# Performance work log

Hardware: AMD Instinct MI355X
Metric: run time of the kernel (lower is better)

## Reference

```python
import jax, jax.numpy as jnp
import numpy as np

B, P, D, N, K = 8, 784, 1536, 20000, 9


def setup_inputs() -> dict:
    key = jax.random.key(0)
    k1, k2 = jax.random.split(key)
    x = jax.random.normal(k1, (B, P, D), dtype=jnp.float32)       # patch embeddings [B, P, D]
    memory = jax.random.normal(k2, (N, D), dtype=jnp.float32)     # FAISS memory bank [N, D]
    return {"x": x, "memory": memory, "k": K}


def reference(x, memory, k):
    # Squared L2 distances (FAISS IndexFlatL2 convention): [B, P, N]
    x2 = jnp.sum(x * x, axis=-1, keepdims=True)                   # [B, P, 1]
    m2 = jnp.sum(memory * memory, axis=-1)                        # [N]
    d = x2 + m2[None, None, :] - 2.0 * jnp.einsum('bpd,nd->bpn', x, memory)
    # k nearest (smallest distances, ascending) -> score_patches [B, P, k]
    neg_topk, _ = jax.lax.top_k(-d, k)
    score_patches = -neg_topk
    closest_dist = score_patches[..., 0]                          # [B, P]
    idxmax = jnp.argmax(closest_dist, axis=1)                     # [B]
    # N_b: the k neighbor distances of the worst (max closest-dist) patch
    N_b = jnp.take_along_axis(score_patches, idxmax[:, None, None], axis=1)[:, 0, :]  # [B, k]
    N_b = N_b - jnp.max(N_b, axis=1, keepdims=True)               # numerical stabilization (as in source)
    N_b_exp = jnp.exp(N_b)
    w = 1.0 - jnp.max(N_b_exp, axis=1) / jnp.sum(N_b_exp, axis=1)  # [B]
    score = w * jnp.max(closest_dist, axis=1)                      # [B]
    return score
```

## Files before the change

### kernel.cpp

```cpp
#include <hip/hip_runtime.h>
#include <hip/hip_fp8.h>
#include <math.h>

#define B_    8
#define P_    784
#define M_    6272
#define D_    1536
#define N_    20000
#define NC_   8

#define MPAD  6400
#define NPAD2 20224
#define MT2   25
#define NT2   79
#define KT2   12

#define NBLK  625

using i32x8  = __attribute__((ext_vector_type(8))) int;
using f32x4v = __attribute__((ext_vector_type(4))) float;

#define GLD_LDS16(src, dst)                                            \
  __builtin_amdgcn_global_load_lds(                                    \
      (__attribute__((address_space(1))) const void*)(src),            \
      (__attribute__((address_space(3))) void*)(dst), 16, 0, 0)

__device__ __forceinline__ unsigned char f2fp8(float v) {
  __hip_fp8_e4m3 q(v);
  return (unsigned char)q.__x;
}

__device__ __forceinline__ unsigned fenc(float f) {
  unsigned u = __float_as_uint(f);
  return (u >> 31) ? ~u : (u | 0x80000000u);
}
__device__ __forceinline__ float fdec(unsigned k) {
  return (k >> 31) ? __uint_as_float(k & 0x7FFFFFFFu) : __uint_as_float(~k);
}

__device__ __forceinline__ void convert_one(const float* __restrict__ src,
                                            unsigned char* __restrict__ dst,
                                            float* __restrict__ sq,
                                            int row, int realrows) {
  const int t = threadIdx.x;
  if (row >= realrows) {
    unsigned* w = (unsigned*)(dst + (size_t)row * D_);
    for (int i = t; i < D_ / 4; i += 256) w[i] = 0u;
    if (t == 0) sq[row] = 1e30f;
    return;
  }
  const float4* r4 = (const float4*)(src + (size_t)row * D_);
  unsigned* w = (unsigned*)(dst + (size_t)row * D_);
  float s = 0.f;
  for (int i = t; i < D_ / 4; i += 256) {
    float4 v = r4[i];
    s += v.x * v.x + v.y * v.y + v.z * v.z + v.w * v.w;
    unsigned pk = (unsigned)f2fp8(v.x) | ((unsigned)f2fp8(v.y) << 8) |
                  ((unsigned)f2fp8(v.z) << 16) | ((unsigned)f2fp8(v.w) << 24);
    w[i] = pk;
  }
#pragma unroll
  for (int m = 32; m >= 1; m >>= 1) s += __shfl_xor(s, m);
  __shared__ float ws4[4];
  if ((t & 63) == 0) ws4[t >> 6] = s;
  __syncthreads();
  if (t == 0) sq[row] = ws4[0] + ws4[1] + ws4[2] + ws4[3];
}

__global__ void convert_all(const float* __restrict__ x, const float* __restrict__ mem,
                            unsigned char* __restrict__ xq, unsigned char* __restrict__ mq,
                            float* __restrict__ x2, float* __restrict__ m2) {
  const int blk = blockIdx.x;
  if (blk < NPAD2) convert_one(mem, mq, m2, blk, N_);
  else convert_one(x, xq, x2, blk - NPAD2, M_);
}

__global__ __launch_bounds__(512, 2) void gemm_min8(
    const unsigned char* __restrict__ xq, const unsigned char* __restrict__ mq,
    const float* __restrict__ m2, unsigned* __restrict__ closest_enc) {
  __shared__ __attribute__((aligned(16))) char ldsFlat[131072];
  __shared__ float ldsMin[4][256];

  const int NWG = MT2 * NT2;
  const int bid = blockIdx.x;
  const int q = NWG >> 3, r = NWG & 7;
  const int xcd = bid & 7, loc = bid >> 3;
  const int wg = (xcd < r ? xcd * (q + 1) : r * (q + 1) + (xcd - r) * q) + loc;
  const int s = wg / (5 * NT2);
  const int r2 = wg - s * (5 * NT2);
  const int mT = s * 5 + (r2 % 5);
  const int nT = r2 / 5;

  const int tid = threadIdx.x;
  const int lane = tid & 63, wid = tid >> 6;
  const int wm = wid >> 2, wn = wid & 3;
  const int g = lane >> 4, r16 = lane & 15;
  const int mBase = mT * 256, nBase = nT * 256;

  const int stRow = wid * 8 + (lane >> 3);
  const int stA = mBase + stRow;
  const int stB = nBase + stRow;
  const int cswz16 = ((lane & 7) ^ ((lane >> 3) & 7)) * 16;

  const int csl = (g * 32) ^ ((r16 & 7) << 4);
  const int csh = csl ^ 16;
  const int rdA = wm * 16384 + r16 * 128;
  const int rdB = wn * 8192 + r16 * 128;

#define STAGE(matsel, srcp, rowb, bufb, h, ktv) do {                        \
    char* dst_ = ldsFlat + (matsel) * 65536 + (bufb) * 32768 +              \
                 (h) * 16384 + wid * 1024;                                  \
    const unsigned char* s_ =                                               \
        (srcp) + (size_t)((rowb) + (h) * 128) * 1536 + (ktv) * 128 + cswz16;\
    GLD_LDS16(s_, dst_);                                                    \
    GLD_LDS16(s_ + 64 * 1536, dst_ + 8192);                                 \
  } while (0)

#define LDFRAG(base, off) ({                                                \
    int4 lo_ = *(const int4*)((base) + (off) + csl);                        \
    int4 hi_ = *(const int4*)((base) + (off) + csh);                        \
    i32x8{lo_.x, lo_.y, lo_.z, lo_.w, hi_.x, hi_.y, hi_.z, hi_.w}; })

#define MFMA8(a, b, c) __builtin_amdgcn_mfma_scale_f32_16x16x128_f8f6f4(    \
    (a), (b), (c), 0, 0, 0, 0x7F7F7F7F, 0, 0x7F7F7F7F)

  f32x4v acc[8][4];
#pragma unroll
  for (int i = 0; i < 8; ++i)
#pragma unroll
    for (int j = 0; j < 4; ++j) acc[i][j] = f32x4v{0.f, 0.f, 0.f, 0.f};

  STAGE(1, mq, stB, 0, 0, 0);
  STAGE(1, mq, stB, 0, 1, 0);
  STAGE(0, xq, stA, 0, 0, 0);
  STAGE(0, xq, stA, 0, 1, 0);
  STAGE(1, mq, stB, 1, 0, 1);
  STAGE(1, mq, stB, 1, 1, 1);
  asm volatile("s_waitcnt vmcnt(4)");
  __builtin_amdgcn_s_barrier();
  __builtin_amdgcn_sched_barrier(0);

#pragma unroll 1
  for (int kt = 0; kt < KT2; ++kt) {
    const int bufc = kt & 1;
    const char* Ab = ldsFlat + bufc * 32768;
    const char* Bb = ldsFlat + 65536 + bufc * 32768;
    const bool stgA = (kt + 1) < KT2;
    const bool stgB = (kt + 2) < KT2;
    i32x8 bf[4], af[4];

#pragma unroll
    for (int nf = 0; nf < 4; ++nf) bf[nf] = LDFRAG(Bb, rdB + nf * 2048);
#pragma unroll
    for (int mf = 0; mf < 4; ++mf) af[mf] = LDFRAG(Ab, rdA + mf * 2048);
    if (stgA) {
      STAGE(0, xq, stA, bufc ^ 1, 0, kt + 1);
      STAGE(0, xq, stA, bufc ^ 1, 1, kt + 1);
    }
    __builtin_amdgcn_s_barrier();
    asm volatile("s_waitcnt lgkmcnt(0)");
    __builtin_amdgcn_s_setprio(1);
#pragma unroll
    for (int mf = 0; mf < 4; ++mf)
#pragma unroll
      for (int nf = 0; nf < 4; ++nf)
        acc[mf][nf] = MFMA8(af[mf], bf[nf], acc[mf][nf]);
    __builtin_amdgcn_s_setprio(0);
    __builtin_amdgcn_s_barrier();

#pragma unroll
    for (int mf = 0; mf < 4; ++mf) af[mf] = LDFRAG(Ab, rdA + (mf + 4) * 2048);
    if (stgB) {
      STAGE(1, mq, stB, bufc, 0, kt + 2);
      STAGE(1, mq, stB, bufc, 1, kt + 2);
    }
    __builtin_amdgcn_s_barrier();
    asm volatile("s_waitcnt lgkmcnt(0)");
    __builtin_amdgcn_s_setprio(1);
#pragma unroll
    for (int mf = 0; mf < 4; ++mf)
#pragma unroll
      for (int nf = 0; nf < 4; ++nf)
        acc[mf + 4][nf] = MFMA8(af[mf], bf[nf], acc[mf + 4][nf]);
    __builtin_amdgcn_s_setprio(0);
    if (kt >= KT2 - 2) {
      asm volatile("s_waitcnt vmcnt(0)");
    } else {
      asm volatile("s_waitcnt vmcnt(4)");
    }
    __builtin_amdgcn_s_barrier();
    __builtin_amdgcn_sched_barrier(0);
  }
#undef STAGE
#undef LDFRAG
#undef MFMA8

  float m2v[4];
#pragma unroll
  for (int nf = 0; nf < 4; ++nf) m2v[nf] = m2[nBase + wn * 64 + nf * 16 + r16];
#pragma unroll
  for (int mf = 0; mf < 8; ++mf) {
    float mn[4];
#pragma unroll
    for (int i = 0; i < 4; ++i) {
      float v = m2v[0] - 2.f * acc[mf][0][i];
      v = fminf(v, m2v[1] - 2.f * acc[mf][1][i]);
      v = fminf(v, m2v[2] - 2.f * acc[mf][2][i]);
      v = fminf(v, m2v[3] - 2.f * acc[mf][3][i]);
      mn[i] = v;
    }
#pragma unroll
    for (int msk = 1; msk < 16; msk <<= 1)
#pragma unroll
      for (int i = 0; i < 4; ++i) mn[i] = fminf(mn[i], __shfl_xor(mn[i], msk));
    if (r16 == 0)
#pragma unroll
      for (int i = 0; i < 4; ++i)
        ldsMin[wn][wm * 128 + mf * 16 + g * 4 + i] = mn[i];
  }
  __syncthreads();
  if (tid < 256) {
    float v = fminf(fminf(ldsMin[0][tid], ldsMin[1][tid]),
                    fminf(ldsMin[2][tid], ldsMin[3][tid]));
    atomicMin(&closest_enc[mBase + tid], fenc(v));
  }
}

__global__ void topcand_kernel(const unsigned* __restrict__ closest_enc,
                               const float* __restrict__ x2,
                               int* __restrict__ cand) {
  const int b = blockIdx.x;
  const int t = threadIdx.x;
  __shared__ float cls[P_];
  for (int p = t; p < P_; p += 256) {
    const int row = b * P_ + p;
    cls[p] = x2[row] + fdec(closest_enc[row]);
  }
  __syncthreads();
  __shared__ float wv[4];
  __shared__ int wi_[4];
  __shared__ int picked[NC_];
  for (int r = 0; r < NC_; ++r) {
    float mv = -3e38f; int mi = 1 << 30;
    for (int p = t; p < P_; p += 256) {
      bool skip = false;
      for (int c = 0; c < r; ++c) skip |= (picked[c] == p);
      float v = cls[p];
      if (!skip && (v > mv || (v == mv && p < mi))) { mv = v; mi = p; }
    }
#pragma unroll
    for (int m = 32; m >= 1; m >>= 1) {
      float ov = __shfl_xor(mv, m); int oi = __shfl_xor(mi, m);
      if (ov > mv || (ov == mv && oi < mi)) { mv = ov; mi = oi; }
    }
    if ((t & 63) == 0) { wv[t >> 6] = mv; wi_[t >> 6] = mi; }
    __syncthreads();
    if (t == 0) {
      float bv = wv[0]; int bi = wi_[0];
      for (int w = 1; w < 4; ++w)
        if (wv[w] > bv || (wv[w] == bv && wi_[w] < bi)) { bv = wv[w]; bi = wi_[w]; }
      picked[r] = bi;
      cand[b * NC_ + r] = bi;
    }
    __syncthreads();
  }
}

__device__ __forceinline__ void ins9(float* t, float v) {
  if (v < t[8]) {
    int p = 8;
    while (p > 0 && t[p - 1] > v) { t[p] = t[p - 1]; --p; }
    t[p] = v;
  }
}

__global__ __launch_bounds__(256) void cand_dist9(
    const float* __restrict__ x, const float* __restrict__ mem,
    const float* __restrict__ x2, const float* __restrict__ m2,
    const int* __restrict__ cand, float* __restrict__ ctop) {
  const int wid = threadIdx.x >> 6, lane = threadIdx.x & 63;
  const int blk = blockIdx.x;
  __shared__ float ldsD[B_ * NC_][36];

  for (int batch = 0; batch < 2; ++batch) {
    const int rbase = blk * 32 + wid * 8 + batch * 4;
    float4 m4[4][6];
    float m2r[4];
#pragma unroll
    for (int k = 0; k < 4; ++k) {
      const float4* mrow = (const float4*)(mem + (size_t)(rbase + k) * D_);
#pragma unroll
      for (int j = 0; j < 6; ++j) m4[k][j] = mrow[j * 64 + lane];
      m2r[k] = m2[rbase + k];
    }
    for (int bc = 0; bc < B_ * NC_; ++bc) {
      const int b = bc / NC_;
      const int p = cand[bc];
      const float4* xp = (const float4*)(x + ((size_t)b * P_ + p) * D_);
      float s0 = 0.f, s1 = 0.f, s2 = 0.f, s3 = 0.f;
#pragma unroll
      for (int j = 0; j < 6; ++j) {
        float4 a = xp[j * 64 + lane];
        s0 += a.x * m4[0][j].x + a.y * m4[0][j].y + a.z * m4[0][j].z + a.w * m4[0][j].w;
        s1 += a.x * m4[1][j].x + a.y * m4[1][j].y + a.z * m4[1][j].z + a.w * m4[1][j].w;
        s2 += a.x * m4[2][j].x + a.y * m4[2][j].y + a.z * m4[2][j].z + a.w * m4[2][j].w;
        s3 += a.x * m4[3][j].x + a.y * m4[3][j].y + a.z * m4[3][j].z + a.w * m4[3][j].w;
      }
#pragma unroll
      for (int msk = 32; msk >= 1; msk >>= 1) {
        s0 += __shfl_xor(s0, msk); s1 += __shfl_xor(s1, msk);
        s2 += __shfl_xor(s2, msk); s3 += __shfl_xor(s3, msk);
      }
      if (lane == 0) {
        const float xx = x2[b * P_ + p];
        const int rloc = wid * 8 + batch * 4;
        ldsD[bc][rloc + 0] = xx + m2r[0] - 2.f * s0;
        ldsD[bc][rloc + 1] = xx + m2r[1] - 2.f * s1;
        ldsD[bc][rloc + 2] = xx + m2r[2] - 2.f * s2;
        ldsD[bc][rloc + 3] = xx + m2r[3] - 2.f * s3;
      }
    }
  }
  __syncthreads();
  if (lane < 16) {
    const int bc = wid * 16 + lane;
    float t[9];
#pragma unroll
    for (int i = 0; i < 9; ++i) t[i] = 3e38f;
    for (int i = 0; i < 32; ++i) ins9(t, ldsD[bc][i]);
    float* o = ctop + ((size_t)bc * NBLK + blk) * 9;
#pragma unroll
    for (int i = 0; i < 9; ++i) o[i] = t[i];
  }
}

__global__ void merge_top9(const float* __restrict__ ctop, float* __restrict__ top9) {
  const int bc = blockIdx.x;
  const float* d = ctop + (size_t)bc * (NBLK * 9);
  float t[9];
#pragma unroll
  for (int i = 0; i < 9; ++i) t[i] = 3e38f;
  for (int n = threadIdx.x; n < NBLK * 9; n += 256) ins9(t, d[n]);
  __shared__ float l9[256 * 9];
  __shared__ float l9b[32 * 9];
  for (int i = 0; i < 9; ++i) l9[threadIdx.x * 9 + i] = t[i];
  __syncthreads();
  if (threadIdx.x < 32) {
    float u[9];
#pragma unroll
    for (int i = 0; i < 9; ++i) u[i] = 3e38f;
    for (int s = 0; s < 8; ++s)
      for (int i = 0; i < 9; ++i) ins9(u, l9[(threadIdx.x * 8 + s) * 9 + i]);
    for (int i = 0; i < 9; ++i) l9b[threadIdx.x * 9 + i] = u[i];
  }
  __syncthreads();
  if (threadIdx.x == 0) {
    float u[9];
#pragma unroll
    for (int i = 0; i < 9; ++i) u[i] = 3e38f;
    for (int s = 0; s < 32; ++s)
      for (int i = 0; i < 9; ++i) ins9(u, l9b[s * 9 + i]);
    for (int i = 0; i < 9; ++i) top9[bc * 9 + i] = u[i];
  }
}

__global__ void score_kernel(const float* __restrict__ top9, const int* __restrict__ cand,
                             float* __restrict__ out) {
  const int b = threadIdx.x;
  if (b >= B_) return;
  float bestv = -3e38f; int bestc = 0, bestp = 1 << 30;
  for (int c = 0; c < NC_; ++c) {
    float v = top9[(b * NC_ + c) * 9 + 0];
    int p = cand[b * NC_ + c];
    if (v > bestv || (v == bestv && p < bestp)) { bestv = v; bestc = c; bestp = p; }
  }
  const float* v9 = &top9[(b * NC_ + bestc) * 9];
  float mx = v9[8];
  float sum = 0.f, mxe = 0.f;
  for (int i = 0; i < 9; ++i) {
    float e = expf(v9[i] - mx);
    sum += e;
    if (e > mxe) mxe = e;
  }
  out[b] = (1.f - mxe / sum) * bestv;
}

extern "C" void kernel_launch(void* const* d_in, const int* in_sizes, int n_in,
                              void* d_out, int out_size, void* d_ws, size_t ws_size,
                              hipStream_t stream) {
  const float* x = (const float*)d_in[0];
  const float* mem = (const float*)d_in[1];
  float* out = (float*)d_out;
  char* ws = (char*)d_ws;

  unsigned char* xq    = (unsigned char*)(ws);
  unsigned char* mq    = (unsigned char*)(ws + 9830400);
  float* x2            = (float*)(ws + 40894464);
  float* m2            = (float*)(ws + 40920064);
  unsigned* closest_enc= (unsigned*)(ws + 41000960);
  int*   cand          = (int*)  (ws + 41026560);
  float* ctop          = (float*)(ws + 41026816);
  float* top9          = (float*)(ws + 42466816);

  hipMemsetAsync(closest_enc, 0xFF, MPAD * 4, stream);
  convert_all<<<NPAD2 + MPAD, 256, 0, stream>>>(x, mem, xq, mq, x2, m2);
  gemm_min8<<<MT2 * NT2, 512, 0, stream>>>(xq, mq, m2, closest_enc);
  topcand_kernel<<<B_, 256, 0, stream>>>(closest_enc, x2, cand);
  cand_dist9<<<NBLK, 256, 0, stream>>>(x, mem, x2, m2, cand, ctop);
  merge_top9<<<B_ * NC_, 256, 0, stream>>>(ctop, top9);
  score_kernel<<<1, 64, 0, stream>>>(top9, cand, out);
}
```

Baseline: 494.5 us.

## Use hardware fp8 pack, fold memset into convert, fuse merge and score

Replaces the per-element fp8 conversion with the packed hardware convert builtin. Folds the closest_enc memset into the convert kernel and merges the top-9 merge and score kernels into one per-batch kernel, removing two launches. Restructures cand_dist9 so each wave holds 8 memory rows in registers at once, so candidate rows are read once instead of twice. In exchange, the fused merge runs only 8 blocks that loop over candidates serially, and cand_dist9 uses more registers.

```diff
diff --git a/kernel.cpp b/kernel.cpp
--- a/kernel.cpp
+++ b/kernel.cpp
@@ -1,5 +1,4 @@
 #include <hip/hip_runtime.h>
-#include <hip/hip_fp8.h>
 #include <math.h>
 
 #define B_    8
@@ -24,11 +23,6 @@
   __builtin_amdgcn_global_load_lds(                                    \
       (__attribute__((address_space(1))) const void*)(src),            \
       (__attribute__((address_space(3))) void*)(dst), 16, 0, 0)
-
-__device__ __forceinline__ unsigned char f2fp8(float v) {
-  __hip_fp8_e4m3 q(v);
-  return (unsigned char)q.__x;
-}
 
 __device__ __forceinline__ unsigned fenc(float f) {
   unsigned u = __float_as_uint(f);
@@ -55,9 +49,9 @@
   for (int i = t; i < D_ / 4; i += 256) {
     float4 v = r4[i];
     s += v.x * v.x + v.y * v.y + v.z * v.z + v.w * v.w;
-    unsigned pk = (unsigned)f2fp8(v.x) | ((unsigned)f2fp8(v.y) << 8) |
-                  ((unsigned)f2fp8(v.z) << 16) | ((unsigned)f2fp8(v.w) << 24);
-    w[i] = pk;
+    int pk = __builtin_amdgcn_cvt_pk_fp8_f32(v.x, v.y, 0, false);
+    pk     = __builtin_amdgcn_cvt_pk_fp8_f32(v.z, v.w, pk, true);
+    w[i] = (unsigned)pk;
   }
 #pragma unroll
   for (int m = 32; m >= 1; m >>= 1) s += __shfl_xor(s, m);
@@ -69,8 +63,11 @@
 
 __global__ void convert_all(const float* __restrict__ x, const float* __restrict__ mem,
                             unsigned char* __restrict__ xq, unsigned char* __restrict__ mq,
-                            float* __restrict__ x2, float* __restrict__ m2) {
+                            float* __restrict__ x2, float* __restrict__ m2,
+                            unsigned* __restrict__ closest_enc) {
   const int blk = blockIdx.x;
+  if (blk < MPAD / 256)
+    closest_enc[blk * 256 + threadIdx.x] = 0xFFFFFFFFu;
   if (blk < NPAD2) convert_one(mem, mq, m2, blk, N_);
   else convert_one(x, xq, x2, blk - NPAD2, M_);
 }
@@ -282,43 +279,40 @@
   const int blk = blockIdx.x;
   __shared__ float ldsD[B_ * NC_][36];
 
-  for (int batch = 0; batch < 2; ++batch) {
-    const int rbase = blk * 32 + wid * 8 + batch * 4;
-    float4 m4[4][6];
-    float m2r[4];
-#pragma unroll
-    for (int k = 0; k < 4; ++k) {
-      const float4* mrow = (const float4*)(mem + (size_t)(rbase + k) * D_);
-#pragma unroll
-      for (int j = 0; j < 6; ++j) m4[k][j] = mrow[j * 64 + lane];
-      m2r[k] = m2[rbase + k];
-    }
-    for (int bc = 0; bc < B_ * NC_; ++bc) {
-      const int b = bc / NC_;
-      const int p = cand[bc];
-      const float4* xp = (const float4*)(x + ((size_t)b * P_ + p) * D_);
-      float s0 = 0.f, s1 = 0.f, s2 = 0.f, s3 = 0.f;
-#pragma unroll
-      for (int j = 0; j < 6; ++j) {
-        float4 a = xp[j * 64 + lane];
-        s0 += a.x * m4[0][j].x + a.y * m4[0][j].y + a.z * m4[0][j].z + a.w * m4[0][j].w;
-        s1 += a.x * m4[1][j].x + a.y * m4[1][j].y + a.z * m4[1][j].z + a.w * m4[1][j].w;
-        s2 += a.x * m4[2][j].x + a.y * m4[2][j].y + a.z * m4[2][j].z + a.w * m4[2][j].w;
-        s3 += a.x * m4[3][j].x + a.y * m4[3][j].y + a.z * m4[3][j].z + a.w * m4[3][j].w;
-      }
-#pragma unroll
-      for (int msk = 32; msk >= 1; msk >>= 1) {
-        s0 += __shfl_xor(s0, msk); s1 += __shfl_xor(s1, msk);
-        s2 += __shfl_xor(s2, msk); s3 += __shfl_xor(s3, msk);
-      }
-      if (lane == 0) {
-        const float xx = x2[b * P_ + p];
-        const int rloc = wid * 8 + batch * 4;
-        ldsD[bc][rloc + 0] = xx + m2r[0] - 2.f * s0;
-        ldsD[bc][rloc + 1] = xx + m2r[1] - 2.f * s1;
-        ldsD[bc][rloc + 2] = xx + m2r[2] - 2.f * s2;
-        ldsD[bc][rloc + 3] = xx + m2r[3] - 2.f * s3;
-      }
+  const int rbase = blk * 32 + wid * 8;
+  float4 m4[8][6];
+  float m2r[8];
+#pragma unroll
+  for (int k = 0; k < 8; ++k) {
+    const float4* mrow = (const float4*)(mem + (size_t)(rbase + k) * D_);
+#pragma unroll
+    for (int j = 0; j < 6; ++j) m4[k][j] = mrow[j * 64 + lane];
+    m2r[k] = m2[rbase + k];
+  }
+#pragma unroll 2
+  for (int bc = 0; bc < B_ * NC_; ++bc) {
+    const int b = bc / NC_;
+    const int p = cand[bc];
+    const float4* xp = (const float4*)(x + ((size_t)b * P_ + p) * D_);
+    float s[8];
+#pragma unroll
+    for (int k = 0; k < 8; ++k) s[k] = 0.f;
+#pragma unroll
+    for (int j = 0; j < 6; ++j) {
+      float4 a = xp[j * 64 + lane];
+#pragma unroll
+      for (int k = 0; k < 8; ++k)
+        s[k] += a.x * m4[k][j].x + a.y * m4[k][j].y + a.z * m4[k][j].z + a.w * m4[k][j].w;
+    }
+#pragma unroll
+    for (int msk = 32; msk >= 1; msk >>= 1)
+#pragma unroll
+      for (int k = 0; k < 8; ++k) s[k] += __shfl_xor(s[k], msk);
+    if (lane == 0) {
+      const float xx = x2[b * P_ + p];
+#pragma unroll
+      for (int k = 0; k < 8; ++k)
+        ldsD[bc][wid * 8 + k] = xx + m2r[k] - 2.f * s[k];
     }
   }
   __syncthreads();
@@ -334,55 +328,57 @@
   }
 }
 
-__global__ void merge_top9(const float* __restrict__ ctop, float* __restrict__ top9) {
-  const int bc = blockIdx.x;
-  const float* d = ctop + (size_t)bc * (NBLK * 9);
-  float t[9];
-#pragma unroll
-  for (int i = 0; i < 9; ++i) t[i] = 3e38f;
-  for (int n = threadIdx.x; n < NBLK * 9; n += 256) ins9(t, d[n]);
+__global__ void merge_score(const float* __restrict__ ctop, const int* __restrict__ cand,
+                            float* __restrict__ out) {
+  const int b = blockIdx.x;
+  const int tid = threadIdx.x;
   __shared__ float l9[256 * 9];
   __shared__ float l9b[32 * 9];
-  for (int i = 0; i < 9; ++i) l9[threadIdx.x * 9 + i] = t[i];
-  __syncthreads();
-  if (threadIdx.x < 32) {
-    float u[9];
-#pragma unroll
-    for (int i = 0; i < 9; ++i) u[i] = 3e38f;
-    for (int s = 0; s < 8; ++s)
-      for (int i = 0; i < 9; ++i) ins9(u, l9[(threadIdx.x * 8 + s) * 9 + i]);
-    for (int i = 0; i < 9; ++i) l9b[threadIdx.x * 9 + i] = u[i];
-  }
-  __syncthreads();
-  if (threadIdx.x == 0) {
-    float u[9];
-#pragma unroll
-    for (int i = 0; i < 9; ++i) u[i] = 3e38f;
-    for (int s = 0; s < 32; ++s)
-      for (int i = 0; i < 9; ++i) ins9(u, l9b[s * 9 + i]);
-    for (int i = 0; i < 9; ++i) top9[bc * 9 + i] = u[i];
-  }
-}
-
-__global__ void score_kernel(const float* __restrict__ top9, const int* __restrict__ cand,
-                             float* __restrict__ out) {
-  const int b = threadIdx.x;
-  if (b >= B_) return;
-  float bestv = -3e38f; int bestc = 0, bestp = 1 << 30;
+  __shared__ float t9[NC_][9];
   for (int c = 0; c < NC_; ++c) {
-    float v = top9[(b * NC_ + c) * 9 + 0];
-    int p = cand[b * NC_ + c];
-    if (v > bestv || (v == bestv && p < bestp)) { bestv = v; bestc = c; bestp = p; }
-  }
-  const float* v9 = &top9[(b * NC_ + bestc) * 9];
-  float mx = v9[8];
-  float sum = 0.f, mxe = 0.f;
-  for (int i = 0; i < 9; ++i) {
-    float e = expf(v9[i] - mx);
-    sum += e;
-    if (e > mxe) mxe = e;
-  }
-  out[b] = (1.f - mxe / sum) * bestv;
+    const float* d = ctop + (size_t)(b * NC_ + c) * (NBLK * 9);
+    float t[9];
+#pragma unroll
+    for (int i = 0; i < 9; ++i) t[i] = 3e38f;
+    for (int n = tid; n < NBLK * 9; n += 256) ins9(t, d[n]);
+    for (int i = 0; i < 9; ++i) l9[tid * 9 + i] = t[i];
+    __syncthreads();
+    if (tid < 32) {
+      float u[9];
+#pragma unroll
+      for (int i = 0; i < 9; ++i) u[i] = 3e38f;
+      for (int s = 0; s < 8; ++s)
+        for (int i = 0; i < 9; ++i) ins9(u, l9[(tid * 8 + s) * 9 + i]);
+      for (int i = 0; i < 9; ++i) l9b[tid * 9 + i] = u[i];
+    }
+    __syncthreads();
+    if (tid == 0) {
+      float u[9];
+#pragma unroll
+      for (int i = 0; i < 9; ++i) u[i] = 3e38f;
+      for (int s = 0; s < 32; ++s)
+        for (int i = 0; i < 9; ++i) ins9(u, l9b[s * 9 + i]);
+      for (int i = 0; i < 9; ++i) t9[c][i] = u[i];
+    }
+    __syncthreads();
+  }
+  if (tid == 0) {
+    float bestv = -3e38f; int bestc = 0, bestp = 1 << 30;
+    for (int c = 0; c < NC_; ++c) {
+      float v = t9[c][0];
+      int p = cand[b * NC_ + c];
+      if (v > bestv || (v == bestv && p < bestp)) { bestv = v; bestc = c; bestp = p; }
+    }
+    const float* v9 = t9[bestc];
+    float mx = v9[8];
+    float sum = 0.f, mxe = 0.f;
+    for (int i = 0; i < 9; ++i) {
+      float e = expf(v9[i] - mx);
+      sum += e;
+      if (e > mxe) mxe = e;
+    }
+    out[b] = (1.f - mxe / sum) * bestv;
+  }
 }
 
 extern "C" void kernel_launch(void* const* d_in, const int* in_sizes, int n_in,
@@ -400,13 +396,10 @@
   unsigned* closest_enc= (unsigned*)(ws + 41000960);
   int*   cand          = (int*)  (ws + 41026560);
   float* ctop          = (float*)(ws + 41026816);
-  float* top9          = (float*)(ws + 42466816);
-
-  hipMemsetAsync(closest_enc, 0xFF, MPAD * 4, stream);
-  convert_all<<<NPAD2 + MPAD, 256, 0, stream>>>(x, mem, xq, mq, x2, m2);
+
+  convert_all<<<NPAD2 + MPAD, 256, 0, stream>>>(x, mem, xq, mq, x2, m2, closest_enc);
   gemm_min8<<<MT2 * NT2, 512, 0, stream>>>(xq, mq, m2, closest_enc);
   topcand_kernel<<<B_, 256, 0, stream>>>(closest_enc, x2, cand);
   cand_dist9<<<NBLK, 256, 0, stream>>>(x, mem, x2, m2, cand, ctop);
-  merge_top9<<<B_ * NC_, 256, 0, stream>>>(ctop, top9);
-  score_kernel<<<1, 64, 0, stream>>>(top9, cand, out);
-}
+  merge_score<<<B_, 256, 0, stream>>>(ctop, cand, out);
+}
```

After: 868.0 us. 1.76x slower.
